# Performance work log

Hardware: AMD Instinct MI355X
Metric: run time of the kernel (lower is better)

Reference implementation:

```python
import jax, jax.numpy as jnp
import numpy as np

N_QUBITS = 6
Q_DEPTH = 2
K = 3
PAD = 1
EPS = 1e-9
Q_DIM = 2 ** N_QUBITS


def _rx(t):
    c = jnp.cos(t / 2).astype(jnp.complex64)
    s = jnp.sin(t / 2).astype(jnp.complex64)
    return jnp.stack([jnp.stack([c, -1j * s]), jnp.stack([-1j * s, c])])


def _ry(t):
    c = jnp.cos(t / 2).astype(jnp.complex64)
    s = jnp.sin(t / 2).astype(jnp.complex64)
    return jnp.stack([jnp.stack([c, -s]), jnp.stack([s, c])])


def _u3(t, p, lm):
    c = jnp.cos(t / 2).astype(jnp.complex64)
    s = jnp.sin(t / 2).astype(jnp.complex64)
    ep = jnp.exp(1j * p.astype(jnp.complex64))
    el = jnp.exp(1j * lm.astype(jnp.complex64))
    return jnp.stack([jnp.stack([c, -el * s]), jnp.stack([ep * s, ep * el * c])])


def _apply_1q(st, U, wire):
    # st: (bsz, 2**n) complex; wire 0 = most significant bit (torchquantum layout)
    s = st.reshape(-1, 2 ** wire, 2, 2 ** (N_QUBITS - wire - 1))
    s = jnp.einsum('ab,nxby->nxay', U, s)
    return s.reshape(-1, Q_DIM)


def _apply_cnot(st, wire):
    # CNOT with control=wire, target=wire+1 (adjacent)
    s = st.reshape(-1, 2 ** wire, 2, 2, 2 ** (N_QUBITS - wire - 2))
    s = jnp.stack([s[:, :, 0], s[:, :, 1, ::-1]], axis=2)
    return s.reshape(-1, Q_DIM)


def _quantum_forward(x, inp_scale, in_proj_w, in_proj_b, weights, meas_w, out_proj_w, out_proj_b):
    B, C, H, W = x.shape
    # Unfold(kernel=3, pad=1, stride=1) -> (B, C*9, H*W), channel-major then (kh, kw)
    xp = jnp.pad(x, ((0, 0), (0, 0), (PAD, PAD), (PAD, PAD)))
    pat = jnp.stack([xp[:, :, i:i + H, j:j + W] for i in range(K) for j in range(K)], axis=2)
    pat = pat.reshape(B, C * K * K, H * W).transpose(0, 2, 1).reshape(-1, C * K * K)
    pf = pat * inp_scale
    xq = pf @ in_proj_w.T + in_proj_b                       # (bsz, 64)
    xq = xq / (jnp.linalg.norm(xq, axis=-1, keepdims=True) + EPS)
    st = xq.astype(jnp.complex64)                           # (bsz, 2**n)
    for l in range(Q_DEPTH):
        for i in range(N_QUBITS):
            st = _apply_1q(st, _rx(weights[l, i, 0]), i)
            st = _apply_1q(st, _ry(weights[l, i, 1]), i)
        for i in range(N_QUBITS - 1):
            st = _apply_cnot(st, i)
        for i in range(N_QUBITS):
            st = _apply_1q(st, _ry(weights[l, i, 2]), i)
    for i in range(N_QUBITS):
        st = _apply_1q(st, _u3(meas_w[i, 0], meas_w[i, 1], meas_w[i, 2]), i)
    probs = st.real ** 2 + st.imag ** 2                     # |amp|^2
    out = probs @ out_proj_w.T + out_proj_b                 # (bsz, out_channels)
    return out.reshape(B, H * W, -1).transpose(0, 2, 1).reshape(B, -1, H, W)


def setup_inputs() -> dict:
    key = jax.random.key(0)
    ks = jax.random.split(key, 8)
    C_IN, C_OUT = 32, 64
    patch_dim = C_IN * K * K  # 288
    x = jax.random.normal(ks[0], (16, C_IN, 64, 64), dtype=jnp.float32)
    inp_scale = jnp.ones((patch_dim,), dtype=jnp.float32)
    in_proj_w = jax.random.normal(ks[1], (Q_DIM, patch_dim), dtype=jnp.float32) / np.sqrt(patch_dim)
    in_proj_b = jax.random.normal(ks[2], (Q_DIM,), dtype=jnp.float32) / np.sqrt(patch_dim)
    weights = 0.1 * jax.random.normal(ks[3], (Q_DEPTH, N_QUBITS, 3), dtype=jnp.float32)
    meas_w = 0.1 * jax.random.normal(ks[4], (N_QUBITS, 3), dtype=jnp.float32)
    out_proj_w = jax.random.normal(ks[5], (C_OUT, Q_DIM), dtype=jnp.float32) / np.sqrt(Q_DIM)
    out_proj_b = jax.random.normal(ks[6], (C_OUT,), dtype=jnp.float32) / np.sqrt(Q_DIM)
    return {"x": x, "inp_scale": inp_scale, "in_proj_w": in_proj_w, "in_proj_b": in_proj_b,
            "weights": weights, "meas_w": meas_w, "out_proj_w": out_proj_w, "out_proj_b": out_proj_b}


def reference(x, inp_scale, in_proj_w, in_proj_b, weights, meas_w, out_proj_w, out_proj_b):
    return _quantum_forward(x, inp_scale, in_proj_w, in_proj_b, weights, meas_w, out_proj_w, out_proj_b)
```

## Files before the change

kernel.cpp:

```cpp
#include <hip/hip_runtime.h>

typedef float f32x4 __attribute__((ext_vector_type(4)));
typedef short bf16x8 __attribute__((ext_vector_type(8)));

#define NB   16
#define CIN  32
#define HW   64
#define CKK  288
#define QD   64

#define WS_WSF 0
#define WS_MCF 18432
#define WS_WOF 26624
#define WS_WEND 30720
#define WS_XQF 30720

__device__ __forceinline__ unsigned short f2bf(float f) {
  unsigned u = __builtin_bit_cast(unsigned, f);
  u += 0x7FFFu + ((u >> 16) & 1u);
  return (unsigned short)(u >> 16);
}

struct C2 { float r, i; };
struct M2 { C2 a, b, c, d; };

__device__ __forceinline__ C2 cmul(C2 x, C2 y) { return { x.r*y.r - x.i*y.i, x.r*y.i + x.i*y.r }; }
__device__ __forceinline__ C2 cadd(C2 x, C2 y) { return { x.r + y.r, x.i + y.i }; }
__device__ __forceinline__ M2 mmul(M2 X, M2 Y) {
  return { cadd(cmul(X.a, Y.a), cmul(X.b, Y.c)),
           cadd(cmul(X.a, Y.b), cmul(X.b, Y.d)),
           cadd(cmul(X.c, Y.a), cmul(X.d, Y.c)),
           cadd(cmul(X.c, Y.b), cmul(X.d, Y.d)) };
}

__device__ __forceinline__ M2 mRX(float t) {
  float s, c; __sincosf(t * 0.5f, &s, &c);
  return { {c,0.f}, {0.f,-s}, {0.f,-s}, {c,0.f} };
}
__device__ __forceinline__ M2 mRY(float t) {
  float s, c; __sincosf(t * 0.5f, &s, &c);
  return { {c,0.f}, {-s,0.f}, {s,0.f}, {c,0.f} };
}
__device__ __forceinline__ M2 mU3(float t, float p, float lm) {
  float s, c; __sincosf(t * 0.5f, &s, &c);
  float sp, cp; __sincosf(p, &sp, &cp);
  float sl, cl; __sincosf(lm, &sl, &cl);
  float spl, cpl; __sincosf(p + lm, &spl, &cpl);
  return { {c,0.f}, {-cl*s, -sl*s}, {cp*s, sp*s}, {cpl*c, spl*c} };
}

__global__ __launch_bounds__(256) void prep_kernel(
    const float* __restrict__ x,
    const float* __restrict__ in_proj_w, const float* __restrict__ inp_scale,
    const float* __restrict__ weights, const float* __restrict__ meas_w,
    const float* __restrict__ out_proj_w, unsigned short* __restrict__ ws)
{
  const int tid = threadIdx.x, blk = blockIdx.x;

  if (blk < 1024) {
    const int b = blk >> 6, y = blk & 63;
    const int lane = tid & 63, w = tid >> 6;
    const float* src = x + ((b * CIN + w * 8) * HW + y) * HW + lane;
    unsigned short* dst = ws + WS_XQF + (size_t)((b * HW + y) * HW + lane) * CIN + w * 8;
    bf16x8 o8;
#pragma unroll
    for (int j = 0; j < 8; ++j) o8[j] = (short)f2bf(src[j * HW * HW]);
    *(bf16x8*)dst = o8;
    return;
  }
  const int blk2 = blk - 1024;

  if (blk2 < 36) {
    int f = blk2, kk = f >> 2, jt = f & 3;
#pragma unroll
    for (int u = 0; u < 2; ++u) {
      int r = tid * 2 + u;
      int lw = r >> 3, e = r & 7;
      int row = jt * 16 + (lw & 15);
      int ch = (lw >> 4) * 8 + e;
      int src = ch * 9 + kk;
      ws[WS_WSF + f * 512 + r] = f2bf(in_proj_w[row * CKK + src] * inp_scale[src]);
    }
    return;
  }
  if (blk2 == 36) {
#pragma unroll
    for (int m = 0; m < 16; ++m) {
      int d = tid * 16 + m;
      int f = d >> 9, r = d & 511;
      int lw = r >> 3, e = r & 7;
      int kk = f >> 2, ot = f & 3;
      int src = (ot * 16 + (lw & 15)) * 64 + kk * 32 + (lw >> 4) * 8 + e;
      ws[WS_WOF + d] = f2bf(out_proj_w[src]);
    }
    return;
  }

  const int lane = tid & 63, wid = tid >> 6;
  const int col = (blk2 - 37) * 4 + wid;

  float re, im;
  {
    C2 amp = {1.f, 0.f};
#pragma unroll
    for (int q = 0; q < 6; ++q) {
      M2 G = mmul(mRY(weights[q * 3 + 1]), mRX(weights[q * 3 + 0]));
      int rb = (lane >> (5 - q)) & 1;
      int cb = (col >> (5 - q)) & 1;
      C2 sel = rb ? (cb ? G.d : G.c) : (cb ? G.b : G.a);
      amp = cmul(amp, sel);
    }
    re = amp.r; im = amp.i;
  }

  const int t1 = (lane ^ (lane >> 1) ^ (lane >> 2) ^ (lane >> 3) ^ (lane >> 4) ^ (lane >> 5)) & 63;
  const int t2 = (lane ^ (lane >> 2) ^ (lane >> 4)) & 63;

  auto applyM = [&](int maskShuf, int rb, M2 U) {
    float arr = rb ? U.d.r : U.a.r, ari = rb ? U.d.i : U.a.i;
    float brr = rb ? U.c.r : U.b.r, bri = rb ? U.c.i : U.b.i;
    float pre = __shfl_xor(re, maskShuf);
    float pim = __shfl_xor(im, maskShuf);
    float nr = arr * re - ari * im + brr * pre - bri * pim;
    float ni = arr * im + ari * re + brr * pim + bri * pre;
    re = nr; im = ni;
  };

  const int MK1[6] = {0x01, 0x03, 0x06, 0x0C, 0x18, 0x30};
  const int MK2[6] = {0x01, 0x02, 0x05, 0x0A, 0x14, 0x28};

#pragma unroll
  for (int q = 0; q < 6; ++q) {
    const int b = 5 - q;
    M2 U = mmul(mmul(mRY(weights[18 + q * 3 + 1]), mRX(weights[18 + q * 3 + 0])),
                mRY(weights[q * 3 + 2]));
    applyM(MK1[b], (t1 >> b) & 1, U);
  }
#pragma unroll
  for (int q = 0; q < 6; ++q) {
    const int b = 5 - q;
    M2 U = mmul(mU3(meas_w[q * 3], meas_w[q * 3 + 1], meas_w[q * 3 + 2]),
                mRY(weights[18 + q * 3 + 2]));
    applyM(MK2[b], (t2 >> b) & 1, U);
  }

  unsigned short* McF = ws + WS_MCF;
  const int nRe = t2 >> 4, c16r = t2 & 15;
  const int kk = col >> 5, gc = (col >> 3) & 3, e = col & 7;
  const int off = (gc * 16 + c16r) * 8 + e;
  McF[(kk * 8 + nRe) * 512 + off]     = f2bf(re);
  McF[(kk * 8 + 4 + nRe) * 512 + off] = f2bf(im);
}

#define LDA 72
#define LDO 65

__global__ __launch_bounds__(512, 4) void main_kernel(
    const float* __restrict__ b_in, const float* __restrict__ b_out,
    const unsigned short* __restrict__ ws, float* __restrict__ out)
{
  __shared__ __align__(16) unsigned char smem[79872];
  unsigned short* w_lds = (unsigned short*)smem;
  unsigned short* a_lds = (unsigned short*)(smem + 61440);
  float* o_lds = (float*)smem;

  const int tid = threadIdx.x, lane = tid & 63, wid = tid >> 6;
  const int g = lane >> 4, c16 = lane & 15;
  const int blk = ((int)blockIdx.x & 7) * 64 + ((int)blockIdx.x >> 3);
  const int b = blk >> 5, h0 = (blk & 31) * 2;
  const int hloc = wid >> 2;
  const int h = h0 + hloc;

  for (int c = tid; c < 3840; c += 512) {
    bf16x8 v = *(const bf16x8*)(ws + c * 8);
    *(bf16x8*)(w_lds + c * 8) = v;
  }
  __syncthreads();

  const unsigned short* WsL = w_lds + WS_WSF;
  const unsigned short* McL = w_lds + WS_MCF;
  const unsigned short* WoL = w_lds + WS_WOF;
  const unsigned short* xqb = ws + WS_XQF + (size_t)b * (HW * HW * CIN);

  f32x4 acc[4];
#pragma unroll
  for (int jt = 0; jt < 4; ++jt) { float bi = b_in[jt * 16 + c16]; acc[jt] = f32x4{bi, bi, bi, bi}; }

  const int ar = (wid & 3) * 16 + c16;
  const int xw0 = (ar >= 1) ? ar - 1 : 0;
  const int xw2 = (ar <= 62) ? ar + 1 : 63;
  const bool ok0 = (ar >= 1), ok2 = (ar <= 62);

#pragma unroll
  for (int kk = 0; kk < 9; ++kk) {
    const int di = kk / 3, dj = kk % 3;
    const int y = h + di - 1;
    bf16x8 af;
    if ((unsigned)y < 64u) {
      const int xwc = (dj == 0) ? xw0 : (dj == 1) ? ar : xw2;
      af = *(const bf16x8*)(xqb + (y * 64 + xwc) * CIN + g * 8);
      const bool okx = (dj == 0) ? ok0 : (dj == 1) ? true : ok2;
      if (!okx)
#pragma unroll
        for (int i = 0; i < 8; ++i) af[i] = 0;
    } else {
#pragma unroll
      for (int i = 0; i < 8; ++i) af[i] = 0;
    }
#pragma unroll
    for (int jt = 0; jt < 4; ++jt) {
      bf16x8 bf_ = *(const bf16x8*)(WsL + (kk * 4 + jt) * 512 + lane * 8);
      acc[jt] = __builtin_amdgcn_mfma_f32_16x16x32_bf16(af, bf_, acc[jt], 0, 0, 0);
    }
  }

  float s[4];
#pragma unroll
  for (int r = 0; r < 4; ++r) {
    float t = acc[0][r] * acc[0][r] + acc[1][r] * acc[1][r] +
              acc[2][r] * acc[2][r] + acc[3][r] * acc[3][r];
    t += __shfl_xor(t, 1); t += __shfl_xor(t, 2); t += __shfl_xor(t, 4); t += __shfl_xor(t, 8);
    s[r] = 1.f / (sqrtf(t) + 1e-9f);
  }
#pragma unroll
  for (int jt = 0; jt < 4; ++jt)
#pragma unroll
    for (int r = 0; r < 4; ++r)
      a_lds[(wid * 16 + g * 4 + r) * LDA + jt * 16 + c16] = f2bf(acc[jt][r] * s[r]);

  f32x4 uv[8];
#pragma unroll
  for (int n = 0; n < 8; ++n) uv[n] = f32x4{0.f, 0.f, 0.f, 0.f};
#pragma unroll
  for (int kk = 0; kk < 2; ++kk) {
    bf16x8 af = *(const bf16x8*)(a_lds + (wid * 16 + c16) * LDA + kk * 32 + g * 8);
#pragma unroll
    for (int n = 0; n < 8; ++n) {
      bf16x8 bf_ = *(const bf16x8*)(McL + (kk * 8 + n) * 512 + lane * 8);
      uv[n] = __builtin_amdgcn_mfma_f32_16x16x32_bf16(af, bf_, uv[n], 0, 0, 0);
    }
  }

#pragma unroll
  for (int n = 0; n < 4; ++n)
#pragma unroll
    for (int r = 0; r < 4; ++r) {
      float p = uv[n][r] * uv[n][r] + uv[n + 4][r] * uv[n + 4][r];
      a_lds[(wid * 16 + g * 4 + r) * LDA + n * 16 + c16] = f2bf(p);
    }

  f32x4 o[4];
#pragma unroll
  for (int ot = 0; ot < 4; ++ot) { float bo = b_out[ot * 16 + c16]; o[ot] = f32x4{bo, bo, bo, bo}; }
#pragma unroll
  for (int kk = 0; kk < 2; ++kk) {
    bf16x8 af = *(const bf16x8*)(a_lds + (wid * 16 + c16) * LDA + kk * 32 + g * 8);
#pragma unroll
    for (int ot = 0; ot < 4; ++ot) {
      bf16x8 bf_ = *(const bf16x8*)(WoL + (kk * 4 + ot) * 512 + lane * 8);
      o[ot] = __builtin_amdgcn_mfma_f32_16x16x32_bf16(af, bf_, o[ot], 0, 0, 0);
    }
  }

  __syncthreads();
#pragma unroll
  for (int ot = 0; ot < 4; ++ot)
#pragma unroll
    for (int r = 0; r < 4; ++r)
      o_lds[hloc * (QD * LDO) + (ot * 16 + c16) * LDO + (wid & 3) * 16 + g * 4 + r] = o[ot][r];
  __syncthreads();

  float* outb = out + (size_t)b * QD * HW * HW + h0 * HW;
#pragma unroll
  for (int it = 0; it < 16; ++it) {
    int r2 = it * 8 + wid;
    int orow = r2 >> 1, hl = r2 & 1;
    outb[orow * (HW * HW) + hl * HW + lane] = o_lds[hl * (QD * LDO) + orow * LDO + lane];
  }
}

extern "C" void kernel_launch(void* const* d_in, const int* in_sizes, int n_in,
                              void* d_out, int out_size, void* d_ws, size_t ws_size,
                              hipStream_t stream) {
  const float* x          = (const float*)d_in[0];
  const float* inp_scale  = (const float*)d_in[1];
  const float* in_proj_w  = (const float*)d_in[2];
  const float* in_proj_b  = (const float*)d_in[3];
  const float* weights    = (const float*)d_in[4];
  const float* meas_w     = (const float*)d_in[5];
  const float* out_proj_w = (const float*)d_in[6];
  const float* out_proj_b = (const float*)d_in[7];
  unsigned short* ws = (unsigned short*)d_ws;

  prep_kernel<<<1077, 256, 0, stream>>>(x, in_proj_w, inp_scale, weights, meas_w, out_proj_w, ws);
  main_kernel<<<512, 512, 0, stream>>>(in_proj_b, out_proj_b, ws, (float*)d_out);
}
```

Baseline: 22.32 us.

## Fuse prep into main kernel, recomputing weights per block and reading x directly

Drops the separate prep kernel. Each block of the main kernel now builds its own bf16 in_proj/out_proj weight fragments and the quantum circuit matrix in LDS. The NCHW fp32 input is read directly with per-channel strided loads and converted to bf16 on the fly, replacing the prior NHWC bf16 transpose through workspace. This removes a kernel launch and a full write-and-read round trip of the activation, but it adds redundant weight and circuit computation in every block and uncoalesced, strided loads across channels.

```diff
diff --git a/kernel.cpp b/kernel.cpp
--- a/kernel.cpp
+++ b/kernel.cpp
@@ -9,11 +9,10 @@
 #define CKK  288
 #define QD   64
 
-#define WS_WSF 0
-#define WS_MCF 18432
-#define WS_WOF 26624
-#define WS_WEND 30720
-#define WS_XQF 30720
+#define L_WSF 0
+#define L_MCF 18432
+#define L_WOF 26624
+#define L_WEND 30720
 
 __device__ __forceinline__ unsigned short f2bf(float f) {
   unsigned u = __builtin_bit_cast(unsigned, f);
@@ -49,115 +48,16 @@
   return { {c,0.f}, {-cl*s, -sl*s}, {cp*s, sp*s}, {cpl*c, spl*c} };
 }
 
-__global__ __launch_bounds__(256) void prep_kernel(
+#define LDA 72
+#define LDO 65
+
+__global__ __launch_bounds__(512, 4) void fused_kernel(
     const float* __restrict__ x,
     const float* __restrict__ in_proj_w, const float* __restrict__ inp_scale,
+    const float* __restrict__ b_in,
     const float* __restrict__ weights, const float* __restrict__ meas_w,
-    const float* __restrict__ out_proj_w, unsigned short* __restrict__ ws)
-{
-  const int tid = threadIdx.x, blk = blockIdx.x;
-
-  if (blk < 1024) {
-    const int b = blk >> 6, y = blk & 63;
-    const int lane = tid & 63, w = tid >> 6;
-    const float* src = x + ((b * CIN + w * 8) * HW + y) * HW + lane;
-    unsigned short* dst = ws + WS_XQF + (size_t)((b * HW + y) * HW + lane) * CIN + w * 8;
-    bf16x8 o8;
-#pragma unroll
-    for (int j = 0; j < 8; ++j) o8[j] = (short)f2bf(src[j * HW * HW]);
-    *(bf16x8*)dst = o8;
-    return;
-  }
-  const int blk2 = blk - 1024;
-
-  if (blk2 < 36) {
-    int f = blk2, kk = f >> 2, jt = f & 3;
-#pragma unroll
-    for (int u = 0; u < 2; ++u) {
-      int r = tid * 2 + u;
-      int lw = r >> 3, e = r & 7;
-      int row = jt * 16 + (lw & 15);
-      int ch = (lw >> 4) * 8 + e;
-      int src = ch * 9 + kk;
-      ws[WS_WSF + f * 512 + r] = f2bf(in_proj_w[row * CKK + src] * inp_scale[src]);
-    }
-    return;
-  }
-  if (blk2 == 36) {
-#pragma unroll
-    for (int m = 0; m < 16; ++m) {
-      int d = tid * 16 + m;
-      int f = d >> 9, r = d & 511;
-      int lw = r >> 3, e = r & 7;
-      int kk = f >> 2, ot = f & 3;
-      int src = (ot * 16 + (lw & 15)) * 64 + kk * 32 + (lw >> 4) * 8 + e;
-      ws[WS_WOF + d] = f2bf(out_proj_w[src]);
-    }
-    return;
-  }
-
-  const int lane = tid & 63, wid = tid >> 6;
-  const int col = (blk2 - 37) * 4 + wid;
-
-  float re, im;
-  {
-    C2 amp = {1.f, 0.f};
-#pragma unroll
-    for (int q = 0; q < 6; ++q) {
-      M2 G = mmul(mRY(weights[q * 3 + 1]), mRX(weights[q * 3 + 0]));
-      int rb = (lane >> (5 - q)) & 1;
-      int cb = (col >> (5 - q)) & 1;
-      C2 sel = rb ? (cb ? G.d : G.c) : (cb ? G.b : G.a);
-      amp = cmul(amp, sel);
-    }
-    re = amp.r; im = amp.i;
-  }
-
-  const int t1 = (lane ^ (lane >> 1) ^ (lane >> 2) ^ (lane >> 3) ^ (lane >> 4) ^ (lane >> 5)) & 63;
-  const int t2 = (lane ^ (lane >> 2) ^ (lane >> 4)) & 63;
-
-  auto applyM = [&](int maskShuf, int rb, M2 U) {
-    float arr = rb ? U.d.r : U.a.r, ari = rb ? U.d.i : U.a.i;
-    float brr = rb ? U.c.r : U.b.r, bri = rb ? U.c.i : U.b.i;
-    float pre = __shfl_xor(re, maskShuf);
-    float pim = __shfl_xor(im, maskShuf);
-    float nr = arr * re - ari * im + brr * pre - bri * pim;
-    float ni = arr * im + ari * re + brr * pim + bri * pre;
-    re = nr; im = ni;
-  };
-
-  const int MK1[6] = {0x01, 0x03, 0x06, 0x0C, 0x18, 0x30};
-  const int MK2[6] = {0x01, 0x02, 0x05, 0x0A, 0x14, 0x28};
-
-#pragma unroll
-  for (int q = 0; q < 6; ++q) {
-    const int b = 5 - q;
-    M2 U = mmul(mmul(mRY(weights[18 + q * 3 + 1]), mRX(weights[18 + q * 3 + 0])),
-                mRY(weights[q * 3 + 2]));
-    applyM(MK1[b], (t1 >> b) & 1, U);
-  }
-#pragma unroll
-  for (int q = 0; q < 6; ++q) {
-    const int b = 5 - q;
-    M2 U = mmul(mU3(meas_w[q * 3], meas_w[q * 3 + 1], meas_w[q * 3 + 2]),
-                mRY(weights[18 + q * 3 + 2]));
-    applyM(MK2[b], (t2 >> b) & 1, U);
-  }
-
-  unsigned short* McF = ws + WS_MCF;
-  const int nRe = t2 >> 4, c16r = t2 & 15;
-  const int kk = col >> 5, gc = (col >> 3) & 3, e = col & 7;
-  const int off = (gc * 16 + c16r) * 8 + e;
-  McF[(kk * 8 + nRe) * 512 + off]     = f2bf(re);
-  McF[(kk * 8 + 4 + nRe) * 512 + off] = f2bf(im);
-}
-
-#define LDA 72
-#define LDO 65
-
-__global__ __launch_bounds__(512, 4) void main_kernel(
-    const float* __restrict__ b_in, const float* __restrict__ b_out,
-    const unsigned short* __restrict__ ws, float* __restrict__ out)
+    const float* __restrict__ out_proj_w, const float* __restrict__ b_out,
+    float* __restrict__ out)
 {
   __shared__ __align__(16) unsigned char smem[79872];
   unsigned short* w_lds = (unsigned short*)smem;
@@ -171,16 +71,105 @@
   const int hloc = wid >> 2;
   const int h = h0 + hloc;
 
-  for (int c = tid; c < 3840; c += 512) {
-    bf16x8 v = *(const bf16x8*)(ws + c * 8);
-    *(bf16x8*)(w_lds + c * 8) = v;
-  }
+  {
+    const int lw = tid >> 3, e = tid & 7;
+    const int r16 = lw & 15, chg = lw >> 4;
+#pragma unroll
+    for (int f = 0; f < 36; ++f) {
+      const int kk = f >> 2, jt = f & 3;
+      const int row = jt * 16 + r16;
+      const int ch = chg * 8 + e;
+      const int src = ch * 9 + kk;
+      w_lds[L_WSF + f * 512 + tid] = f2bf(in_proj_w[row * CKK + src] * inp_scale[src]);
+    }
+#pragma unroll
+    for (int f = 0; f < 8; ++f) {
+      const int kk = f >> 2, ot = f & 3;
+      const int src = (ot * 16 + r16) * 64 + kk * 32 + chg * 8 + e;
+      w_lds[L_WOF + f * 512 + tid] = f2bf(out_proj_w[src]);
+    }
+  }
+
+  {
+    C2 e0[6], e1[6];
+#pragma unroll
+    for (int q = 0; q < 6; ++q) {
+      M2 G = mmul(mRY(weights[q * 3 + 1]), mRX(weights[q * 3 + 0]));
+      int rb = (lane >> (5 - q)) & 1;
+      e0[q] = rb ? G.c : G.a;
+      e1[q] = rb ? G.d : G.b;
+    }
+    const int colbase = wid * 8;
+    float re[8], im[8];
+#pragma unroll
+    for (int j = 0; j < 8; ++j) {
+      const int col = colbase + j;
+      C2 amp = {1.f, 0.f};
+#pragma unroll
+      for (int q = 0; q < 6; ++q) {
+        int cb = (col >> (5 - q)) & 1;
+        C2 sel = cb ? e1[q] : e0[q];
+        amp = cmul(amp, sel);
+      }
+      re[j] = amp.r; im[j] = amp.i;
+    }
+
+    const int t1 = (lane ^ (lane >> 1) ^ (lane >> 2) ^ (lane >> 3) ^ (lane >> 4) ^ (lane >> 5)) & 63;
+    const int t2 = (lane ^ (lane >> 2) ^ (lane >> 4)) & 63;
+    const int MK1[6] = {0x01, 0x03, 0x06, 0x0C, 0x18, 0x30};
+    const int MK2[6] = {0x01, 0x02, 0x05, 0x0A, 0x14, 0x28};
+
+#pragma unroll
+    for (int q = 0; q < 6; ++q) {
+      const int bb = 5 - q;
+      M2 U = mmul(mmul(mRY(weights[18 + q * 3 + 1]), mRX(weights[18 + q * 3 + 0])),
+                  mRY(weights[q * 3 + 2]));
+      const int rb = (t1 >> bb) & 1;
+      const float arr = rb ? U.d.r : U.a.r, ari = rb ? U.d.i : U.a.i;
+      const float brr = rb ? U.c.r : U.b.r, bri = rb ? U.c.i : U.b.i;
+#pragma unroll
+      for (int j = 0; j < 8; ++j) {
+        float pre = __shfl_xor(re[j], MK1[bb]);
+        float pim = __shfl_xor(im[j], MK1[bb]);
+        float nr = arr * re[j] - ari * im[j] + brr * pre - bri * pim;
+        float ni = arr * im[j] + ari * re[j] + brr * pim + bri * pre;
+        re[j] = nr; im[j] = ni;
+      }
+    }
+#pragma unroll
+    for (int q = 0; q < 6; ++q) {
+      const int bb = 5 - q;
+      M2 U = mmul(mU3(meas_w[q * 3], meas_w[q * 3 + 1], meas_w[q * 3 + 2]),
+                  mRY(weights[18 + q * 3 + 2]));
+      const int rb = (t2 >> bb) & 1;
+      const float arr = rb ? U.d.r : U.a.r, ari = rb ? U.d.i : U.a.i;
+      const float brr = rb ? U.c.r : U.b.r, bri = rb ? U.c.i : U.b.i;
+#pragma unroll
+      for (int j = 0; j < 8; ++j) {
+        float pre = __shfl_xor(re[j], MK2[bb]);
+        float pim = __shfl_xor(im[j], MK2[bb]);
+        float nr = arr * re[j] - ari * im[j] + brr * pre - bri * pim;
+        float ni = arr * im[j] + ari * re[j] + brr * pim + bri * pre;
+        re[j] = nr; im[j] = ni;
+      }
+    }
+
+    const int nRe = t2 >> 4, c16r = t2 & 15;
+#pragma unroll
+    for (int j = 0; j < 8; ++j) {
+      const int col = colbase + j;
+      const int kk = col >> 5, gc = (col >> 3) & 3, e = col & 7;
+      const int off = (gc * 16 + c16r) * 8 + e;
+      w_lds[L_MCF + (kk * 8 + nRe) * 512 + off]     = f2bf(re[j]);
+      w_lds[L_MCF + (kk * 8 + 4 + nRe) * 512 + off] = f2bf(im[j]);
+    }
+  }
+
   __syncthreads();
 
-  const unsigned short* WsL = w_lds + WS_WSF;
-  const unsigned short* McL = w_lds + WS_MCF;
-  const unsigned short* WoL = w_lds + WS_WOF;
-  const unsigned short* xqb = ws + WS_XQF + (size_t)b * (HW * HW * CIN);
+  const unsigned short* WsL = w_lds + L_WSF;
+  const unsigned short* McL = w_lds + L_MCF;
+  const unsigned short* WoL = w_lds + L_WOF;
 
   f32x4 acc[4];
 #pragma unroll
@@ -190,6 +179,7 @@
   const int xw0 = (ar >= 1) ? ar - 1 : 0;
   const int xw2 = (ar <= 62) ? ar + 1 : 63;
   const bool ok0 = (ar >= 1), ok2 = (ar <= 62);
+  const float* xb = x + b * CIN * HW * HW;
 
 #pragma unroll
   for (int kk = 0; kk < 9; ++kk) {
@@ -198,11 +188,14 @@
     bf16x8 af;
     if ((unsigned)y < 64u) {
       const int xwc = (dj == 0) ? xw0 : (dj == 1) ? ar : xw2;
-      af = *(const bf16x8*)(xqb + (y * 64 + xwc) * CIN + g * 8);
       const bool okx = (dj == 0) ? ok0 : (dj == 1) ? true : ok2;
-      if (!okx)
-#pragma unroll
-        for (int i = 0; i < 8; ++i) af[i] = 0;
+      const float* py = xb + y * 64 + xwc;
+#pragma unroll
+      for (int i = 0; i < 8; ++i) {
+        float v = py[(g * 8 + i) * 4096];
+        v = okx ? v : 0.f;
+        af[i] = (short)f2bf(v);
+      }
     } else {
 #pragma unroll
       for (int i = 0; i < 8; ++i) af[i] = 0;
@@ -290,8 +283,8 @@
   const float* meas_w     = (const float*)d_in[5];
   const float* out_proj_w = (const float*)d_in[6];
   const float* out_proj_b = (const float*)d_in[7];
-  unsigned short* ws = (unsigned short*)d_ws;
-
-  prep_kernel<<<1077, 256, 0, stream>>>(x, in_proj_w, inp_scale, weights, meas_w, out_proj_w, ws);
-  main_kernel<<<512, 512, 0, stream>>>(in_proj_b, out_proj_b, ws, (float*)d_out);
-}
+
+  fused_kernel<<<512, 512, 0, stream>>>(x, in_proj_w, inp_scale, in_proj_b,
+                                        weights, meas_w, out_proj_w, out_proj_b,
+                                        (float*)d_out);
+}
```

Result: slower. 32.53 us (+45.7%).
